# Optimization experiments

Hardware: AMD Instinct MI355X
Metric: run time of the kernel (lower is better)

## Reference

```python
import jax, jax.numpy as jnp
import numpy as np

B, C, N = 4, 512, 2048
H, DK = 8, 64  # n_heads, d_k; H*DK == C


def setup_inputs() -> dict:
    key = jax.random.key(0)
    k1, k2, k3 = jax.random.split(key, 3)
    x = jax.random.normal(k1, (B, C, N), dtype=jnp.float32)
    # Linear(C, 3*H*DK) and Linear(H*DK, C); torch Linear weight is [out, in]
    Wp = jax.random.normal(k2, (3 * H * DK, C), dtype=jnp.float32) * (C ** -0.5)
    bp = jnp.zeros((3 * H * DK,), dtype=jnp.float32)
    Wo = jax.random.normal(k3, (C, H * DK), dtype=jnp.float32) * ((H * DK) ** -0.5)
    bo = jnp.zeros((C,), dtype=jnp.float32)
    return {"x": x, "Wp": Wp, "bp": bp, "Wo": Wo, "bo": bo}


def reference(x, Wp, bp, Wo, bo):
    b, c, n = x.shape
    scale = DK ** -0.5
    xt = jnp.transpose(x, (0, 2, 1))                    # [b, n, c]
    # NOTE: original forward never applies self.norm (GroupNorm) — faithful omission.
    qkv = xt @ Wp.T + bp                                # [b, n, 3*H*DK]
    qkv = qkv.reshape(b, n, H, 3 * DK)
    q, k, v = jnp.split(qkv, 3, axis=-1)                # each [b, n, H, DK]
    attn = jnp.einsum('bihd,bjhd->bijh', q, k) * scale  # [b, n, n, H]
    attn = jax.nn.softmax(attn, axis=1)                 # softmax over QUERY axis (nonstandard)
    res = jnp.einsum('bijh,bjhd->bihd', attn, v)        # [b, n, H, DK]
    res = res.reshape(b, n, H * DK)
    res = res @ Wo.T + bo                               # [b, n, c]
    res = res + xt                                      # shortcut = Identity (in==out)
    return jnp.transpose(res, (0, 2, 1)).reshape(b, c, n)
```

## Files before the change

kernel.cpp:

```cpp
#include <hip/hip_runtime.h>
#include <cstddef>

typedef unsigned short ushort_t;
typedef __attribute__((ext_vector_type(8))) short sh8;
typedef __attribute__((ext_vector_type(4))) float f4;
typedef __attribute__((ext_vector_type(4))) unsigned short us4;

static constexpr int Bc = 4, Cc = 512, Nc = 2048, Hc = 8, DKc = 64, O3c = 1536;
static constexpr int BHN = Bc * Hc * Nc;
static constexpr int NSPLIT_S = 2;
static constexpr float K2 = 0.125f * 1.44269504089f;

__device__ __forceinline__ unsigned short f2bf(float f) {
    union { float f; unsigned u; } v; v.f = f;
    unsigned r = v.u + 0x7FFFu + ((v.u >> 16) & 1u);
    return (unsigned short)(r >> 16);
}
__device__ __forceinline__ float bf2f(unsigned short b) {
    union { unsigned u; float f; } v; v.u = ((unsigned)b) << 16;
    return v.f;
}
__device__ __forceinline__ float ubf(unsigned u) {
    union { unsigned u; float f; } v; v.u = u; return v.f;
}
__device__ __forceinline__ float fexp2(float s) {
    return ubf((unsigned)(int)fmaf(s, 8388608.0f, 1065353216.0f));
}
__device__ __forceinline__ int fexp2_bf(float s) {
    return (int)fmaf(s, 128.0f, 16256.5f);
}
__device__ __forceinline__ void gl_lds16(const ushort_t* g, ushort_t* l) {
    __builtin_amdgcn_global_load_lds(
        (const __attribute__((address_space(1))) unsigned int*)g,
        (__attribute__((address_space(3))) unsigned int*)l, 16, 0, 0);
}

__global__ __launch_bounds__(256) void xpose_kernel(
    const float* __restrict__ x, ushort_t* __restrict__ xt)
{
    __shared__ float t[32][33];
    const int b = blockIdx.z, n0 = blockIdx.x * 32, c0 = blockIdx.y * 32;
    const int tx = threadIdx.x & 31, ty = threadIdx.x >> 5;
    const float* xb = x + (size_t)b * Cc * Nc;
#pragma unroll
    for (int r = 0; r < 4; ++r)
        t[ty + r * 8][tx] = xb[(size_t)(c0 + ty + r * 8) * Nc + n0 + tx];
    __syncthreads();
    ushort_t* xtb = xt + (size_t)b * Nc * Cc;
#pragma unroll
    for (int r = 0; r < 4; ++r)
        xtb[(size_t)(n0 + ty + r * 8) * Cc + c0 + tx] = f2bf(t[tx][ty + r * 8]);
}

__global__ __launch_bounds__(256) void cvt_kernel(
    const float* __restrict__ s, ushort_t* __restrict__ d, int n4)
{
    int i = blockIdx.x * 256 + threadIdx.x;
    if (i < n4) {
        float4 v = ((const float4*)s)[i];
        us4 o = { f2bf(v.x), f2bf(v.y), f2bf(v.z), f2bf(v.w) };
        ((us4*)d)[i] = o;
    }
}

__global__ __launch_bounds__(256, 2) void qkv_kernel(
    const ushort_t* __restrict__ xt, const ushort_t* __restrict__ Wpb,
    const float* __restrict__ bp,
    ushort_t* __restrict__ q, ushort_t* __restrict__ k, ushort_t* __restrict__ vT)
{
    __shared__ __align__(16) ushort_t As[128 * 64];
    __shared__ __align__(16) ushort_t Bs[128 * 64];
    const int tid = threadIdx.x;
    const int wave = tid >> 6, lane = tid & 63, quad = lane >> 4, l15 = lane & 15;
    const int b = blockIdx.z;
    const int t0  = blockIdx.y * 128;
    const int o0b = blockIdx.x * 128;
    const int wt = wave & 1, wo = wave >> 1;
    const int m0 = t0 + wt * 64;
    const int o0 = o0b + wo * 64;
    const ushort_t* Ag = xt  + ((size_t)b * Nc + t0) * Cc;
    const ushort_t* Bg = Wpb + (size_t)o0b * Cc;
    const int f  = (o0 >> 6) % 3;
    const int h  = o0 / 192;
    const int bh = b * Hc + h;
    const int sw = l15 & 7;

    f4 acc[4][4];
#pragma unroll
    for (int i = 0; i < 4; ++i)
#pragma unroll
        for (int j = 0; j < 4; ++j) acc[i][j] = (f4)0.f;

    int goff[4], lbase[4];
#pragma unroll
    for (int c = 0; c < 4; ++c) {
        int g = c * 256 + tid;
        int r = g >> 3, cn = (g & 7) ^ (r & 7);
        goff[c]  = r * Cc + cn * 8;
        lbase[c] = (c * 256 + wave * 64) * 8;
    }

    for (int st = 0; st < 8; ++st) {
        const int k0 = st * 64;
#pragma unroll
        for (int c = 0; c < 4; ++c) {
            gl_lds16(Ag + k0 + goff[c], As + lbase[c]);
            gl_lds16(Bg + k0 + goff[c], Bs + lbase[c]);
        }
        __syncthreads();

        sh8 aA[4][2], bB[4][2];
#pragma unroll
        for (int mi = 0; mi < 4; ++mi)
#pragma unroll
            for (int kk = 0; kk < 2; ++kk)
                aA[mi][kk] = *(const sh8*)&As[(wt * 64 + mi * 16 + l15) * 64 +
                                              (((kk * 4 + quad) ^ sw) << 3)];
#pragma unroll
        for (int ni = 0; ni < 4; ++ni)
#pragma unroll
            for (int kk = 0; kk < 2; ++kk)
                bB[ni][kk] = *(const sh8*)&Bs[(wo * 64 + ni * 16 + l15) * 64 +
                                              (((kk * 4 + quad) ^ sw) << 3)];
        if (f == 2) {
#pragma unroll
            for (int kk = 0; kk < 2; ++kk)
#pragma unroll
                for (int mi = 0; mi < 4; ++mi)
#pragma unroll
                    for (int ni = 0; ni < 4; ++ni)
                        acc[mi][ni] = __builtin_amdgcn_mfma_f32_16x16x32_bf16(
                            aA[mi][kk], bB[ni][kk], acc[mi][ni], 0, 0, 0);
        } else {
#pragma unroll
            for (int kk = 0; kk < 2; ++kk)
#pragma unroll
                for (int mo = 0; mo < 4; ++mo)
#pragma unroll
                    for (int nt = 0; nt < 4; ++nt)
                        acc[mo][nt] = __builtin_amdgcn_mfma_f32_16x16x32_bf16(
                            bB[mo][kk], aA[nt][kk], acc[mo][nt], 0, 0, 0);
        }
        __syncthreads();
    }

    if (f == 2) {
#pragma unroll
        for (int ni = 0; ni < 4; ++ni) {
            const int o = o0 + ni * 16 + l15;
            const int d = o & 63;
            const float bias = bp[o];
            ushort_t* dst = vT + ((size_t)bh * DKc + d) * Nc + m0;
#pragma unroll
            for (int mi = 0; mi < 4; ++mi) {
                us4 pk = { f2bf(acc[mi][ni][0] + bias), f2bf(acc[mi][ni][1] + bias),
                           f2bf(acc[mi][ni][2] + bias), f2bf(acc[mi][ni][3] + bias) };
                *(us4*)&dst[mi * 16 + quad * 4] = pk;
            }
        }
    } else {
        const float qs = (f == 0) ? K2 : 1.0f;
        ushort_t* dst = (f == 0 ? q : k) + (size_t)bh * Nc * DKc;
#pragma unroll
        for (int mo = 0; mo < 4; ++mo) {
            const int d0 = mo * 16 + quad * 4;
            const float4 b4 = *(const float4*)&bp[o0 + d0];
#pragma unroll
            for (int nt = 0; nt < 4; ++nt) {
                const int token = m0 + nt * 16 + l15;
                us4 pk = { f2bf((acc[mo][nt][0] + b4.x) * qs),
                           f2bf((acc[mo][nt][1] + b4.y) * qs),
                           f2bf((acc[mo][nt][2] + b4.z) * qs),
                           f2bf((acc[mo][nt][3] + b4.w) * qs) };
                *(us4*)&dst[(size_t)token * DKc + d0] = pk;
            }
        }
    }
}

__global__ __launch_bounds__(256, 2) void stats_kernel(
    const ushort_t* __restrict__ q, const ushort_t* __restrict__ k,
    float* __restrict__ spart)
{
    const int tid = threadIdx.x;
    const int wave = tid >> 6, lane = tid & 63, quad = lane >> 4, l15 = lane & 15;
    const int id = blockIdx.x;
    const int jb = id >> 6;
    const int bh = (id & 63) >> 1;
    const int js = id & 1;
    const int j0 = jb * 256 + wave * 64;
    const int ibase = js * (Nc / NSPLIT_S);
    const ushort_t* K = k + ((size_t)bh * Nc + j0) * DKc;
    const ushort_t* Q = q + (size_t)bh * Nc * DKc;

    sh8 aK[4][2];
#pragma unroll
    for (int mj = 0; mj < 4; ++mj)
#pragma unroll
        for (int kk = 0; kk < 2; ++kk)
            aK[mj][kk] = *(const sh8*)&K[(size_t)(mj * 16 + l15) * DKc + kk * 32 + quad * 8];

    float lsum[4][4] = {};
    for (int it = 0; it < Nc / NSPLIT_S; it += 64) {
        const int i0 = ibase + it;
        sh8 bQ[4][2];
#pragma unroll
        for (int ni = 0; ni < 4; ++ni)
#pragma unroll
            for (int kk = 0; kk < 2; ++kk)
                bQ[ni][kk] = *(const sh8*)&Q[(size_t)(i0 + ni * 16 + l15) * DKc + kk * 32 + quad * 8];
#pragma unroll
        for (int mj = 0; mj < 4; ++mj)
#pragma unroll
            for (int ni = 0; ni < 4; ++ni) {
                f4 s = (f4)0.f;
                s = __builtin_amdgcn_mfma_f32_16x16x32_bf16(aK[mj][0], bQ[ni][0], s, 0, 0, 0);
                s = __builtin_amdgcn_mfma_f32_16x16x32_bf16(aK[mj][1], bQ[ni][1], s, 0, 0, 0);
#pragma unroll
                for (int r = 0; r < 4; ++r)
                    lsum[mj][r] += fexp2(s[r]);
            }
    }
#pragma unroll
    for (int mj = 0; mj < 4; ++mj)
#pragma unroll
        for (int r = 0; r < 4; ++r) {
            float v = lsum[mj][r];
            v += __shfl_xor(v, 1); v += __shfl_xor(v, 2);
            v += __shfl_xor(v, 4); v += __shfl_xor(v, 8);
            if (l15 == 0)
                spart[((size_t)js * Bc * Hc + bh) * Nc + j0 + mj * 16 + quad * 4 + r] = v;
        }
}

__global__ __launch_bounds__(256) void vscale_kernel(
    ushort_t* __restrict__ vT, const float* __restrict__ spart)
{
    int i = blockIdx.x * 256 + threadIdx.x;
    int f = i * 4;
    int row = f >> 11;
    int j = f & 2047;
    int bh = row >> 6;
    const float* sp = spart + (size_t)bh * Nc + j;
    float4 s0 = *(const float4*)sp;
    float4 s1 = *(const float4*)(sp + BHN);
    us4 v = ((us4*)vT)[i];
    us4 o = { f2bf(bf2f(v[0]) / (s0.x + s1.x)), f2bf(bf2f(v[1]) / (s0.y + s1.y)),
              f2bf(bf2f(v[2]) / (s0.z + s1.z)), f2bf(bf2f(v[3]) / (s0.w + s1.w)) };
    ((us4*)vT)[i] = o;
}

__global__ __launch_bounds__(256, 2) void apply_kernel(
    const ushort_t* __restrict__ q, const ushort_t* __restrict__ k,
    const ushort_t* __restrict__ vT,
    ushort_t* __restrict__ part0, ushort_t* __restrict__ part1)
{
    __shared__ __align__(16) ushort_t Ks[128 * 64];
    __shared__ __align__(16) ushort_t Vs[64 * 128];
    __shared__ __align__(16) ushort_t Ps[4][64 * 64];
    const int tid = threadIdx.x;
    const int wave = tid >> 6, lane = tid & 63, quad = lane >> 4, l15 = lane & 15;
    const int id = blockIdx.x;
    const int ibk = id >> 6;
    const int bh = (id & 63) >> 1;
    const int js = id & 1;
    const int b = bh >> 3, h = bh & 7;
    const int i0 = ibk * 256 + wave * 64;
    const int jbase = js * (Nc / 2);
    const ushort_t* Q  = q  + ((size_t)bh * Nc + i0) * DKc;
    const ushort_t* Kb = k  + (size_t)bh * Nc * DKc;
    const ushort_t* Vb = vT + (size_t)bh * DKc * Nc;
    ushort_t* Pw = Ps[wave];
    const int sw = l15 & 7;
    const int hb = (l15 >> 3) & 1;

    sh8 bQ[4][2];
#pragma unroll
    for (int ni = 0; ni < 4; ++ni)
#pragma unroll
        for (int kk = 0; kk < 2; ++kk)
            bQ[ni][kk] = *(const sh8*)&Q[(size_t)(ni * 16 + l15) * DKc + kk * 32 + quad * 8];

    f4 acc[4][4];
#pragma unroll
    for (int i = 0; i < 4; ++i)
#pragma unroll
        for (int j = 0; j < 4; ++j) acc[i][j] = (f4)0.f;

    int koff[4], voff[4], lbase[4];
#pragma unroll
    for (int c = 0; c < 4; ++c) {
        int g = c * 256 + tid;
        int rk = g >> 3, ck = (g & 7) ^ (rk & 7);
        koff[c] = rk * DKc + ck * 8;
        int rv = g >> 4, cs = g & 15, cn = (cs & 8) | ((cs & 7) ^ (rv & 7));
        voff[c] = rv * Nc + cn * 8;
        lbase[c] = (c * 256 + wave * 64) * 8;
    }

    for (int st = 0; st < 8; ++st) {
        const int j0 = jbase + st * 128;
#pragma unroll
        for (int c = 0; c < 4; ++c) {
            gl_lds16(Kb + (size_t)j0 * DKc + koff[c], Ks + lbase[c]);
            gl_lds16(Vb + voff[c] + j0,               Vs + lbase[c]);
        }
        __syncthreads();

#pragma unroll
        for (int jj = 0; jj < 128; jj += 64) {
            sh8 aK[4][2];
#pragma unroll
            for (int mj = 0; mj < 4; ++mj)
#pragma unroll
                for (int kk = 0; kk < 2; ++kk)
                    aK[mj][kk] = *(const sh8*)&Ks[(jj + mj * 16 + l15) * 64 +
                                                  (((kk * 4 + quad) ^ sw) << 3)];
#pragma unroll
            for (int ni = 0; ni < 4; ++ni) {
                const int prow = ni * 16 + l15;
#pragma unroll
                for (int mj = 0; mj < 4; ++mj) {
                    f4 s = (f4)0.f;
                    s = __builtin_amdgcn_mfma_f32_16x16x32_bf16(aK[mj][0], bQ[ni][0], s, 0, 0, 0);
                    s = __builtin_amdgcn_mfma_f32_16x16x32_bf16(aK[mj][1], bQ[ni][1], s, 0, 0, 0);
                    const int e0 = fexp2_bf(s[0]);
                    const int e1 = fexp2_bf(s[1]);
                    const int e2 = fexp2_bf(s[2]);
                    const int e3 = fexp2_bf(s[3]);
                    uint2 pk;
                    pk.x = __builtin_amdgcn_perm((unsigned)e1, (unsigned)e0, 0x05040100u);
                    pk.y = __builtin_amdgcn_perm((unsigned)e3, (unsigned)e2, 0x05040100u);
                    const int off = prow * 64 + ((((mj * 2 + (quad >> 1)) ^ sw)) << 3)
                                  + (((quad & 1) ^ hb) << 2);
                    *(uint2*)&Pw[off] = pk;
                }
            }
#pragma unroll
            for (int kk = 0; kk < 2; ++kk) {
                const int cgk = (((kk * 4 + quad) ^ sw)) << 3;
                const int h0 = hb << 2, h1 = 4 - h0;
                sh8 aP[4], bV[4];
#pragma unroll
                for (int mi = 0; mi < 4; ++mi) {
                    union { sh8 s8; uint2 u[2]; } t;
                    const int rb = (mi * 16 + l15) * 64 + cgk;
                    t.u[0] = *(const uint2*)&Pw[rb + h0];
                    t.u[1] = *(const uint2*)&Pw[rb + h1];
                    aP[mi] = t.s8;
                }
                const int gnat = (jj >> 3) + kk * 4 + quad;
                const int vcg = ((gnat & 8) | ((gnat & 7) ^ sw)) << 3;
#pragma unroll
                for (int nd = 0; nd < 4; ++nd)
                    bV[nd] = *(const sh8*)&Vs[(nd * 16 + l15) * 128 + vcg];
#pragma unroll
                for (int mi = 0; mi < 4; ++mi)
#pragma unroll
                    for (int nd = 0; nd < 4; ++nd)
                        acc[mi][nd] = __builtin_amdgcn_mfma_f32_16x16x32_bf16(
                            aP[mi], bV[nd], acc[mi][nd], 0, 0, 0);
            }
        }
        __syncthreads();
    }

    ushort_t* part = js ? part1 : part0;
    ushort_t* dst = part + ((size_t)b * Nc + i0) * Cc + h * DKc;
#pragma unroll
    for (int mi = 0; mi < 4; ++mi)
#pragma unroll
        for (int nd = 0; nd < 4; ++nd)
#pragma unroll
            for (int r = 0; r < 4; ++r)
                dst[(size_t)(mi * 16 + quad * 4 + r) * Cc + nd * 16 + l15] =
                    f2bf(acc[mi][nd][r]);
}

__global__ __launch_bounds__(256) void reduce_kernel(
    const ushort_t* __restrict__ p0, ushort_t* __restrict__ p1res)
{
    int i = blockIdx.x * 256 + threadIdx.x;
    us4 a = ((const us4*)p0)[i];
    us4 b = ((const us4*)p1res)[i];
    us4 o;
#pragma unroll
    for (int j = 0; j < 4; ++j)
        o[j] = f2bf(bf2f(a[j]) + bf2f(b[j]));
    ((us4*)p1res)[i] = o;
}

__global__ __launch_bounds__(256) void out_kernel(
    const ushort_t* __restrict__ res, const ushort_t* __restrict__ Wob,
    const float* __restrict__ bo, const float* __restrict__ x,
    float* __restrict__ out)
{
    const int tid = threadIdx.x;
    const int wave = tid >> 6, lane = tid & 63, quad = lane >> 4, l15 = lane & 15;
    const int m0  = blockIdx.x * 128 + (wave & 1) * 64;
    const int co0 = blockIdx.y * 128 + (wave >> 1) * 64;
    const ushort_t* A  = res + (size_t)m0 * Cc;
    const ushort_t* Bw = Wob + (size_t)co0 * Cc;

    f4 acc[4][4];
#pragma unroll
    for (int i = 0; i < 4; ++i)
#pragma unroll
        for (int j = 0; j < 4; ++j) acc[i][j] = (f4)0.f;

    for (int kk = 0; kk < Cc; kk += 32) {
        sh8 a[4], bb[4];
#pragma unroll
        for (int mi = 0; mi < 4; ++mi)
            a[mi] = *(const sh8*)&A[(size_t)(mi * 16 + l15) * Cc + kk + quad * 8];
#pragma unroll
        for (int ni = 0; ni < 4; ++ni)
            bb[ni] = *(const sh8*)&Bw[(size_t)(ni * 16 + l15) * Cc + kk + quad * 8];
#pragma unroll
        for (int mi = 0; mi < 4; ++mi)
#pragma unroll
            for (int ni = 0; ni < 4; ++ni)
                acc[mi][ni] = __builtin_amdgcn_mfma_f32_16x16x32_bf16(
                    a[mi], bb[ni], acc[mi][ni], 0, 0, 0);
    }

    const int b = m0 >> 11;
    const int n_base = m0 & 2047;
#pragma unroll
    for (int ni = 0; ni < 4; ++ni) {
        const int co = co0 + ni * 16 + l15;
        const float bias = bo[co];
#pragma unroll
        for (int mi = 0; mi < 4; ++mi) {
            const int n = n_base + mi * 16 + quad * 4;
            const size_t idx = ((size_t)b * Cc + co) * Nc + n;
            float4 xr = *(const float4*)&x[idx];
            float4 o;
            o.x = acc[mi][ni][0] + bias + xr.x;
            o.y = acc[mi][ni][1] + bias + xr.y;
            o.z = acc[mi][ni][2] + bias + xr.z;
            o.w = acc[mi][ni][3] + bias + xr.w;
            *(float4*)&out[idx] = o;
        }
    }
}

extern "C" void kernel_launch(void* const* d_in, const int* in_sizes, int n_in,
                              void* d_out, int out_size, void* d_ws, size_t ws_size,
                              hipStream_t stream)
{
    const float* x  = (const float*)d_in[0];
    const float* Wp = (const float*)d_in[1];
    const float* bp = (const float*)d_in[2];
    const float* Wo = (const float*)d_in[3];
    const float* bo = (const float*)d_in[4];
    float* out = (float*)d_out;

    float* coef  = (float*)d_ws;
    float* spart = coef + BHN;
    ushort_t* wsb = (ushort_t*)(spart + (size_t)NSPLIT_S * BHN);
    const size_t nE = (size_t)Bc * Nc * Cc;
    ushort_t* xt  = wsb;
    ushort_t* Wpb = xt  + nE;
    ushort_t* Wob = Wpb + (size_t)O3c * Cc;
    ushort_t* qw  = Wob + (size_t)Cc * Cc;
    ushort_t* kw  = qw + nE;
    ushort_t* vT  = kw + nE;
    ushort_t* res = vT + nE;

    xpose_kernel<<<dim3(Nc / 32, Cc / 32, Bc), 256, 0, stream>>>(x, xt);
    cvt_kernel<<<dim3((O3c * Cc / 4 + 255) / 256), 256, 0, stream>>>(Wp, Wpb, O3c * Cc / 4);
    cvt_kernel<<<dim3((Cc * Cc / 4 + 255) / 256), 256, 0, stream>>>(Wo, Wob, Cc * Cc / 4);
    qkv_kernel<<<dim3(O3c / 128, Nc / 128, Bc), 256, 0, stream>>>(xt, Wpb, bp, qw, kw, vT);
    stats_kernel<<<dim3(512), 256, 0, stream>>>(qw, kw, spart);
    vscale_kernel<<<dim3((int)(nE / 4 / 256)), 256, 0, stream>>>(vT, spart);
    apply_kernel<<<dim3(512), 256, 0, stream>>>(qw, kw, vT, xt, res);
    reduce_kernel<<<dim3((int)(nE / 4 / 256)), 256, 0, stream>>>(xt, res);
    out_kernel<<<dim3(Bc * Nc / 128, Cc / 128), 256, 0, stream>>>(res, Wob, bo, x, out);
}
```

Baseline: 202.6 us.

## Split stats over four query chunks, merge weight casts, LDS-tile output GEMM

```diff
diff --git a/kernel.cpp b/kernel.cpp
--- a/kernel.cpp
+++ b/kernel.cpp
@@ -8,7 +8,7 @@
 
 static constexpr int Bc = 4, Cc = 512, Nc = 2048, Hc = 8, DKc = 64, O3c = 1536;
 static constexpr int BHN = Bc * Hc * Nc;
-static constexpr int NSPLIT_S = 2;
+static constexpr int NSPLIT_S = 4;
 static constexpr float K2 = 0.125f * 1.44269504089f;
 
 __device__ __forceinline__ unsigned short f2bf(float f) {
@@ -52,15 +52,15 @@
         xtb[(size_t)(n0 + ty + r * 8) * Cc + c0 + tx] = f2bf(t[tx][ty + r * 8]);
 }
 
-__global__ __launch_bounds__(256) void cvt_kernel(
-    const float* __restrict__ s, ushort_t* __restrict__ d, int n4)
+__global__ __launch_bounds__(256) void cvt2_kernel(
+    const float* __restrict__ s1, const float* __restrict__ s2,
+    ushort_t* __restrict__ d, int n4a, int n4tot)
 {
     int i = blockIdx.x * 256 + threadIdx.x;
-    if (i < n4) {
-        float4 v = ((const float4*)s)[i];
-        us4 o = { f2bf(v.x), f2bf(v.y), f2bf(v.z), f2bf(v.w) };
-        ((us4*)d)[i] = o;
-    }
+    if (i >= n4tot) return;
+    float4 v = (i < n4a) ? ((const float4*)s1)[i] : ((const float4*)s2)[i - n4a];
+    us4 o = { f2bf(v.x), f2bf(v.y), f2bf(v.z), f2bf(v.w) };
+    ((us4*)d)[i] = o;
 }
 
 __global__ __launch_bounds__(256, 2) void qkv_kernel(
@@ -178,18 +178,18 @@
     }
 }
 
-__global__ __launch_bounds__(256, 2) void stats_kernel(
+__global__ __launch_bounds__(256, 4) void stats_kernel(
     const ushort_t* __restrict__ q, const ushort_t* __restrict__ k,
     float* __restrict__ spart)
 {
     const int tid = threadIdx.x;
     const int wave = tid >> 6, lane = tid & 63, quad = lane >> 4, l15 = lane & 15;
     const int id = blockIdx.x;
-    const int jb = id >> 6;
-    const int bh = (id & 63) >> 1;
-    const int js = id & 1;
+    const int jb = id >> 7;
+    const int bh = (id >> 2) & 31;
+    const int is = id & 3;
     const int j0 = jb * 256 + wave * 64;
-    const int ibase = js * (Nc / NSPLIT_S);
+    const int ibase = is * (Nc / NSPLIT_S);
     const ushort_t* K = k + ((size_t)bh * Nc + j0) * DKc;
     const ushort_t* Q = q + (size_t)bh * Nc * DKc;
 
@@ -229,7 +229,7 @@
             v += __shfl_xor(v, 1); v += __shfl_xor(v, 2);
             v += __shfl_xor(v, 4); v += __shfl_xor(v, 8);
             if (l15 == 0)
-                spart[((size_t)js * Bc * Hc + bh) * Nc + j0 + mj * 16 + quad * 4 + r] = v;
+                spart[((size_t)is * Bc * Hc + bh) * Nc + j0 + mj * 16 + quad * 4 + r] = v;
         }
 }
 
@@ -244,9 +244,13 @@
     const float* sp = spart + (size_t)bh * Nc + j;
     float4 s0 = *(const float4*)sp;
     float4 s1 = *(const float4*)(sp + BHN);
+    float4 s2 = *(const float4*)(sp + 2 * BHN);
+    float4 s3 = *(const float4*)(sp + 3 * BHN);
+    float4 t = { s0.x + s1.x + s2.x + s3.x, s0.y + s1.y + s2.y + s3.y,
+                 s0.z + s1.z + s2.z + s3.z, s0.w + s1.w + s2.w + s3.w };
     us4 v = ((us4*)vT)[i];
-    us4 o = { f2bf(bf2f(v[0]) / (s0.x + s1.x)), f2bf(bf2f(v[1]) / (s0.y + s1.y)),
-              f2bf(bf2f(v[2]) / (s0.z + s1.z)), f2bf(bf2f(v[3]) / (s0.w + s1.w)) };
+    us4 o = { f2bf(bf2f(v[0]) / t.x), f2bf(bf2f(v[1]) / t.y),
+              f2bf(bf2f(v[2]) / t.z), f2bf(bf2f(v[3]) / t.w) };
     ((us4*)vT)[i] = o;
 }
 
@@ -390,45 +394,83 @@
     ((us4*)p1res)[i] = o;
 }
 
-__global__ __launch_bounds__(256) void out_kernel(
+__global__ __launch_bounds__(256, 2) void out_kernel(
     const ushort_t* __restrict__ res, const ushort_t* __restrict__ Wob,
     const float* __restrict__ bo, const float* __restrict__ x,
     float* __restrict__ out)
 {
+    __shared__ __align__(16) ushort_t As[128 * 64];
+    __shared__ __align__(16) ushort_t Bs[64 * 64];
     const int tid = threadIdx.x;
     const int wave = tid >> 6, lane = tid & 63, quad = lane >> 4, l15 = lane & 15;
-    const int m0  = blockIdx.x * 128 + (wave & 1) * 64;
-    const int co0 = blockIdx.y * 128 + (wave >> 1) * 64;
-    const ushort_t* A  = res + (size_t)m0 * Cc;
-    const ushort_t* Bw = Wob + (size_t)co0 * Cc;
-
-    f4 acc[4][4];
+    const int wt = wave & 1, wo = wave >> 1;
+    const int t0   = blockIdx.x * 128;
+    const int co0b = blockIdx.y * 64;
+    const ushort_t* Ag = res + (size_t)t0 * Cc;
+    const ushort_t* Bg = Wob + (size_t)co0b * Cc;
+    const int sw = l15 & 7;
+
+    f4 acc[4][2];
 #pragma unroll
     for (int i = 0; i < 4; ++i)
 #pragma unroll
-        for (int j = 0; j < 4; ++j) acc[i][j] = (f4)0.f;
-
-    for (int kk = 0; kk < Cc; kk += 32) {
-        sh8 a[4], bb[4];
+        for (int j = 0; j < 2; ++j) acc[i][j] = (f4)0.f;
+
+    int goffA[4], lbaseA[4], goffB[2], lbaseB[2];
+#pragma unroll
+    for (int c = 0; c < 4; ++c) {
+        int g = c * 256 + tid;
+        int r = g >> 3, cn = (g & 7) ^ (r & 7);
+        goffA[c]  = r * Cc + cn * 8;
+        lbaseA[c] = (c * 256 + wave * 64) * 8;
+    }
+#pragma unroll
+    for (int c = 0; c < 2; ++c) {
+        int g = c * 256 + tid;
+        int r = g >> 3, cn = (g & 7) ^ (r & 7);
+        goffB[c]  = r * Cc + cn * 8;
+        lbaseB[c] = (c * 256 + wave * 64) * 8;
+    }
+
+    for (int st = 0; st < 8; ++st) {
+        const int k0 = st * 64;
+#pragma unroll
+        for (int c = 0; c < 4; ++c)
+            gl_lds16(Ag + k0 + goffA[c], As + lbaseA[c]);
+#pragma unroll
+        for (int c = 0; c < 2; ++c)
+            gl_lds16(Bg + k0 + goffB[c], Bs + lbaseB[c]);
+        __syncthreads();
+
+        sh8 aA[4][2], bB[2][2];
 #pragma unroll
         for (int mi = 0; mi < 4; ++mi)
-            a[mi] = *(const sh8*)&A[(size_t)(mi * 16 + l15) * Cc + kk + quad * 8];
-#pragma unroll
-        for (int ni = 0; ni < 4; ++ni)
-            bb[ni] = *(const sh8*)&Bw[(size_t)(ni * 16 + l15) * Cc + kk + quad * 8];
-#pragma unroll
-        for (int mi = 0; mi < 4; ++mi)
-#pragma unroll
-            for (int ni = 0; ni < 4; ++ni)
-                acc[mi][ni] = __builtin_amdgcn_mfma_f32_16x16x32_bf16(
-                    a[mi], bb[ni], acc[mi][ni], 0, 0, 0);
-    }
-
-    const int b = m0 >> 11;
-    const int n_base = m0 & 2047;
-#pragma unroll
-    for (int ni = 0; ni < 4; ++ni) {
-        const int co = co0 + ni * 16 + l15;
+#pragma unroll
+            for (int kk = 0; kk < 2; ++kk)
+                aA[mi][kk] = *(const sh8*)&As[(wt * 64 + mi * 16 + l15) * 64 +
+                                              (((kk * 4 + quad) ^ sw) << 3)];
+#pragma unroll
+        for (int ni = 0; ni < 2; ++ni)
+#pragma unroll
+            for (int kk = 0; kk < 2; ++kk)
+                bB[ni][kk] = *(const sh8*)&Bs[(wo * 32 + ni * 16 + l15) * 64 +
+                                              (((kk * 4 + quad) ^ sw) << 3)];
+#pragma unroll
+        for (int kk = 0; kk < 2; ++kk)
+#pragma unroll
+            for (int mi = 0; mi < 4; ++mi)
+#pragma unroll
+                for (int ni = 0; ni < 2; ++ni)
+                    acc[mi][ni] = __builtin_amdgcn_mfma_f32_16x16x32_bf16(
+                        aA[mi][kk], bB[ni][kk], acc[mi][ni], 0, 0, 0);
+        __syncthreads();
+    }
+
+    const int b = t0 >> 11;
+    const int n_base = (t0 & 2047) + wt * 64;
+#pragma unroll
+    for (int ni = 0; ni < 2; ++ni) {
+        const int co = co0b + wo * 32 + ni * 16 + l15;
         const float bias = bo[co];
 #pragma unroll
         for (int mi = 0; mi < 4; ++mi) {
@@ -468,13 +510,15 @@
     ushort_t* vT  = kw + nE;
     ushort_t* res = vT + nE;
 
+    const int n4a   = O3c * Cc / 4;
+    const int n4tot = n4a + Cc * Cc / 4;
+
     xpose_kernel<<<dim3(Nc / 32, Cc / 32, Bc), 256, 0, stream>>>(x, xt);
-    cvt_kernel<<<dim3((O3c * Cc / 4 + 255) / 256), 256, 0, stream>>>(Wp, Wpb, O3c * Cc / 4);
-    cvt_kernel<<<dim3((Cc * Cc / 4 + 255) / 256), 256, 0, stream>>>(Wo, Wob, Cc * Cc / 4);
+    cvt2_kernel<<<dim3(n4tot / 256), 256, 0, stream>>>(Wp, Wo, Wpb, n4a, n4tot);
     qkv_kernel<<<dim3(O3c / 128, Nc / 128, Bc), 256, 0, stream>>>(xt, Wpb, bp, qw, kw, vT);
-    stats_kernel<<<dim3(512), 256, 0, stream>>>(qw, kw, spart);
+    stats_kernel<<<dim3(1024), 256, 0, stream>>>(qw, kw, spart);
     vscale_kernel<<<dim3((int)(nE / 4 / 256)), 256, 0, stream>>>(vT, spart);
     apply_kernel<<<dim3(512), 256, 0, stream>>>(qw, kw, vT, xt, res);
     reduce_kernel<<<dim3((int)(nE / 4 / 256)), 256, 0, stream>>>(xt, res);
-    out_kernel<<<dim3(Bc * Nc / 128, Cc / 128), 256, 0, stream>>>(res, Wob, bo, x, out);
-}
+    out_kernel<<<dim3(Bc * Nc / 128, Cc / 64), 256, 0, stream>>>(res, Wob, bo, x, out);
+}
```

Result: no change. 200.2 us (-1.2%).
